# Kernel tuning notes

Hardware: AMD Instinct MI355X
Metric: run time of the kernel (lower is better)

Reference implementation:

```python
import jax, jax.numpy as jnp
import numpy as np

B, D, R = 16384, 4096, 64       # batch tokens, embed_dim, low_rank_dimension
N_PART = 8                       # number of subspace partitions
P = R // N_PART                  # partition size = 8
N_SEL = 4                        # partitions selected per example


def setup_inputs() -> dict:
    key = jax.random.key(0)
    k1, k2, k3, k4 = jax.random.split(key, 4)
    base = jax.random.normal(k1, (B, D), dtype=jnp.float32)
    source = jax.random.normal(k2, (B, D), dtype=jnp.float32)
    # orthogonal low-rank rotation (torch.nn.utils.parametrizations.orthogonal)
    W, _ = jnp.linalg.qr(jax.random.normal(k3, (D, R), dtype=jnp.float32))  # [D, R], orthonormal cols
    subspaces = jax.random.randint(k4, (B, N_SEL), 0, N_PART)               # partition ids per example
    return {"base": base, "source": source, "W": W, "subspaces": subspaces}


def reference(base, source, W, subspaces):
    # rotate into low-rank space: [B, R]
    rotated_base = base @ W
    rotated_source = source @ W
    diff = rotated_source - rotated_base

    # per-example selected rotated-space indices (contiguous partitions of size P)
    # idx[b] = concat over selected partitions of [p*P, p*P+P)
    idx = (subspaces[:, :, None] * P + jnp.arange(P)).reshape(B, N_SEL * P)  # [B, N_SEL*P]

    # Selecting columns of diff and matching rows of W.T, then matmul, is
    # equivalent to masking unselected rotated dims to zero and doing one GEMM.
    mask = jnp.zeros((B, R), dtype=diff.dtype).at[jnp.arange(B)[:, None], idx].set(1.0)
    output = base + (diff * mask) @ W.T  # [B, D]
    return output.astype(base.dtype)
```

## Files before the change

kernel.cpp:

```cpp
#include <hip/hip_runtime.h>


#define D_DIM 4096
#define R_DIM 64
#define BM    32
#define WAVESTG 16384
#define K1_SMEM 65536
#define OFF_RM  65536
#define FUSED_SMEM 70144

typedef short bf16vec8 __attribute__((ext_vector_type(8)));
typedef float f32x4v  __attribute__((ext_vector_type(4)));

#define VMWAIT(N)                                              \
  do {                                                         \
    asm volatile("s_waitcnt vmcnt(" #N ")" ::: "memory");      \
    __builtin_amdgcn_sched_barrier(0);                         \
  } while (0)

__device__ __forceinline__ unsigned int f2bf_u(float f) {
  unsigned int u = __builtin_bit_cast(unsigned int, f);
  return (u + 0x7fffu + ((u >> 16) & 1u)) >> 16;
}
__device__ __forceinline__ unsigned int pack2bf(float a, float b) {
  return f2bf_u(a) | (f2bf_u(b) << 16);
}
__device__ __forceinline__ void async_ld16(const void* g, void* l) {
  __builtin_amdgcn_global_load_lds(
      (const __attribute__((address_space(1))) void*)g,
      (__attribute__((address_space(3))) void*)l, 16, 0, 0);
}

__global__ __launch_bounds__(256)
void lrri_prep(const float* __restrict__ W, unsigned short* __restrict__ Wt,
               unsigned short* __restrict__ Wb) {
  const int idx = blockIdx.x * blockDim.x + threadIdx.x;
  const int k = idx >> 4;
  const int j = (idx & 15) * 4;
  float4 w = *(const float4*)(W + (size_t)k * R_DIM + j);
  ushort4 p;
  p.x = (unsigned short)f2bf_u(w.x);
  p.y = (unsigned short)f2bf_u(w.y);
  p.z = (unsigned short)f2bf_u(w.z);
  p.w = (unsigned short)f2bf_u(w.w);
  *(ushort4*)(Wb + (size_t)k * R_DIM + j) = p;
  Wt[(size_t)(j + 0) * D_DIM + k] = p.x;
  Wt[(size_t)(j + 1) * D_DIM + k] = p.y;
  Wt[(size_t)(j + 2) * D_DIM + k] = p.z;
  Wt[(size_t)(j + 3) * D_DIM + k] = p.w;
}

__global__ __launch_bounds__(256, 2)
void k1_rotdiff(const float* __restrict__ base, const float* __restrict__ srcp,
                const int* __restrict__ subs,
                const unsigned short* __restrict__ Wt_bf,
                unsigned short* __restrict__ rm_g)
{
  __shared__ __align__(16) unsigned char smem[K1_SMEM];
  const int tid  = threadIdx.x;
  const int wave = tid >> 6;
  const int lane = tid & 63;
  const int l4   = lane & 15;
  const int g    = lane >> 4;
  const int rh   = wave >> 1;
  const int kh   = wave & 1;
  const long rowbase = (long)blockIdx.x * BM;
  const long rowg    = rowbase + rh * 16;
  unsigned char* wbuf = smem + wave * WAVESTG;
  const int off1 = (blockIdx.x * 7) & 63;

  f32x4v acc[4];
  #pragma unroll
  for (int t = 0; t < 4; ++t) acc[t] = (f32x4v){0.f, 0.f, 0.f, 0.f};

  auto stage = [&](int c) {
    const int ch = (c + off1) & 63;
    unsigned char* buf = wbuf + (c & 1) * 8192;
    const long colf = kh * 2048 + ch * 32;
    #pragma unroll
    for (int q = 0; q < 2; ++q) {
      const int r = q * 8 + (lane >> 3);
      const unsigned b = ((unsigned)((lane & 7) * 16)) ^ ((unsigned)(r & 7) << 4);
      const long goff = (rowg + r) * (long)D_DIM + colf + (b >> 2);
      async_ld16(base + goff, buf + q * 1024);
    }
    #pragma unroll
    for (int q = 0; q < 2; ++q) {
      const int r = q * 8 + (lane >> 3);
      const unsigned b = ((unsigned)((lane & 7) * 16)) ^ ((unsigned)(r & 7) << 4);
      const long goff = (rowg + r) * (long)D_DIM + colf + (b >> 2);
      async_ld16(srcp + goff, buf + 2048 + q * 1024);
    }
    #pragma unroll
    for (int q = 0; q < 4; ++q) {
      const int j = q * 16 + (lane >> 2);
      const unsigned kb = ((unsigned)((lane & 3) * 16)) ^ ((unsigned)(j & 3) << 4);
      const char* src = (const char*)Wt_bf + (size_t)j * (D_DIM * 2) +
                        colf * 2 + kb;
      async_ld16(src, buf + 4096 + q * 1024);
    }
  };

  auto compute = [&](int c) {
    const unsigned char* buf = wbuf + (c & 1) * 8192;
    const unsigned sw = (unsigned)((l4 & 7) << 4);
    const unsigned c0 = ((unsigned)(g * 32)) ^ sw;
    const unsigned c1 = ((unsigned)(g * 32 + 16)) ^ sw;
    float4 fb0 = *(const float4*)(buf + l4 * 128 + c0);
    float4 fb1 = *(const float4*)(buf + l4 * 128 + c1);
    float4 fs0 = *(const float4*)(buf + 2048 + l4 * 128 + c0);
    float4 fs1 = *(const float4*)(buf + 2048 + l4 * 128 + c1);
    uint4 af;
    af.x = pack2bf(fs0.x - fb0.x, fs0.y - fb0.y);
    af.y = pack2bf(fs0.z - fb0.z, fs0.w - fb0.w);
    af.z = pack2bf(fs1.x - fb1.x, fs1.y - fb1.y);
    af.w = pack2bf(fs1.z - fb1.z, fs1.w - fb1.w);
    const unsigned wsl = ((unsigned)(g * 16)) ^ ((unsigned)(l4 & 3) << 4);
    #pragma unroll
    for (int t = 0; t < 4; ++t) {
      uint4 wf = *(const uint4*)(buf + 4096 + (t * 16 + l4) * 64 + wsl);
      acc[t] = __builtin_amdgcn_mfma_f32_16x16x32_bf16(
          __builtin_bit_cast(bf16vec8, af),
          __builtin_bit_cast(bf16vec8, wf), acc[t], 0, 0, 0);
    }
  };

  stage(0); stage(1);
  #pragma unroll 1
  for (int c = 0; c < 62; ++c) {
    VMWAIT(8);
    compute(c);
    __builtin_amdgcn_sched_barrier(0);
    stage(c + 2);
  }
  VMWAIT(8);
  compute(62);
  VMWAIT(0);
  compute(63);

  {
    float* part = (float*)wbuf;
    #pragma unroll
    for (int t = 0; t < 4; ++t)
      #pragma unroll
      for (int i = 0; i < 4; ++i)
        part[(g * 4 + i) * 72 + t * 16 + l4] = acc[t][i];
  }
  __syncthreads();

  {
    const int row = tid >> 3, jg = tid & 7;
    const int lr  = row & 15;
    const float* pa = (const float*)(smem + ((row >> 4) * 2 + 0) * WAVESTG);
    const float* pb = (const float*)(smem + ((row >> 4) * 2 + 1) * WAVESTG);
    int4 sb = *(const int4*)(subs + (rowbase + row) * 4);
    unsigned mbits = (1u << sb.x) | (1u << sb.y) | (1u << sb.z) | (1u << sb.w);
    unsigned short v[8];
    #pragma unroll
    for (int jj = 0; jj < 8; ++jj) {
      const int j = jg * 8 + jj;
      float sum = pa[lr * 72 + j] + pb[lr * 72 + j];
      v[jj] = ((mbits >> (j >> 3)) & 1u) ? (unsigned short)f2bf_u(sum)
                                         : (unsigned short)0;
    }
    uint4 pk;
    pk.x = (unsigned)v[0] | ((unsigned)v[1] << 16);
    pk.y = (unsigned)v[2] | ((unsigned)v[3] << 16);
    pk.z = (unsigned)v[4] | ((unsigned)v[5] << 16);
    pk.w = (unsigned)v[6] | ((unsigned)v[7] << 16);
    *(uint4*)(rm_g + (rowbase + row) * 64 + jg * 8) = pk;
  }
}

__global__ __launch_bounds__(256, 4)
void k2_apply(const float* __restrict__ base,
              const unsigned short* __restrict__ rm_g,
              const unsigned short* __restrict__ Wb_bf,
              float* __restrict__ out)
{
  __shared__ __align__(16) unsigned char smem[36864];
  const int tid  = threadIdx.x;
  const int wave = tid >> 6;
  const int lane = tid & 63;
  const int l4   = lane & 15;
  const int g    = lane >> 4;
  const long rowbase = (long)blockIdx.x * BM;
  const int off2 = (blockIdx.x * 5) & 15;

  uint4 a2[2][2];
  #pragma unroll
  for (int m = 0; m < 2; ++m)
    #pragma unroll
    for (int s = 0; s < 2; ++s)
      a2[m][s] = *(const uint4*)(rm_g + (rowbase + m * 16 + l4) * 64 +
                                 s * 32 + g * 8);

  float* cbuf = (float*)(smem + wave * 9216);
  #pragma unroll 1
  for (int grp = 0; grp < 16; ++grp) {
    const int ga = (grp + off2) & 15;
    const int cbase = wave * 1024 + ga * 64;
    float4 bb[8];
    #pragma unroll
    for (int v2 = 0; v2 < 8; ++v2) {
      const int r = g + v2 * 4;
      bb[v2] = *(const float4*)(base + (rowbase + r) * D_DIM + cbase + l4 * 4);
    }
    f32x4v a[2][4];
    #pragma unroll
    for (int m = 0; m < 2; ++m)
      #pragma unroll
      for (int t = 0; t < 4; ++t) a[m][t] = (f32x4v){0.f, 0.f, 0.f, 0.f};
    #pragma unroll
    for (int t = 0; t < 4; ++t) {
      #pragma unroll
      for (int s = 0; s < 2; ++s) {
        uint4 bfrag = *(const uint4*)(Wb_bf +
            (size_t)(cbase + t * 16 + l4) * R_DIM + s * 32 + g * 8);
        #pragma unroll
        for (int m = 0; m < 2; ++m)
          a[m][t] = __builtin_amdgcn_mfma_f32_16x16x32_bf16(
              __builtin_bit_cast(bf16vec8, a2[m][s]),
              __builtin_bit_cast(bf16vec8, bfrag), a[m][t], 0, 0, 0);
      }
    }
    #pragma unroll
    for (int m = 0; m < 2; ++m)
      #pragma unroll
      for (int t = 0; t < 4; ++t)
        #pragma unroll
        for (int i = 0; i < 4; ++i)
          cbuf[(m * 16 + g * 4 + i) * 72 + t * 16 + l4] = a[m][t][i];
    __syncthreads();
    #pragma unroll
    for (int v2 = 0; v2 < 8; ++v2) {
      const int r = g + v2 * 4;
      f32x4v cv = *(const f32x4v*)(cbuf + r * 72 + l4 * 4);
      float4 o;
      o.x = cv[0] + bb[v2].x;
      o.y = cv[1] + bb[v2].y;
      o.z = cv[2] + bb[v2].z;
      o.w = cv[3] + bb[v2].w;
      *(float4*)(out + (rowbase + r) * D_DIM + cbase + l4 * 4) = o;
    }
    __syncthreads();
  }
}

__global__ __launch_bounds__(256, 2)
void lrri_fused_nows(const float* __restrict__ base, const float* __restrict__ srcp,
                     const float* __restrict__ W, const int* __restrict__ subs,
                     float* __restrict__ out)
{
  __shared__ __align__(16) unsigned char smem[FUSED_SMEM];
  const int tid  = threadIdx.x;
  const int wave = tid >> 6;
  const int lane = tid & 63;
  const int l4   = lane & 15;
  const int g    = lane >> 4;
  const int rh   = wave >> 1;
  const int kh   = wave & 1;
  const long rowbase = (long)blockIdx.x * BM;
  const long rowg    = rowbase + rh * 16;
  unsigned char* wbuf = smem + wave * WAVESTG;
  const int off1 = (blockIdx.x * 7) & 63;
  const int off2 = (blockIdx.x * 5) & 15;

  f32x4v acc[4];
  #pragma unroll
  for (int t = 0; t < 4; ++t) acc[t] = (f32x4v){0.f, 0.f, 0.f, 0.f};

  #pragma unroll 1
  for (int c = 0; c < 64; ++c) {
    const int ch = (c + off1) & 63;
    unsigned char* buf = wbuf + (c & 1) * 8192;
    const long colf = kh * 2048 + ch * 32;
    #pragma unroll
    for (int q = 0; q < 2; ++q) {
      const int r = q * 8 + (lane >> 3);
      const unsigned b = ((unsigned)((lane & 7) * 16)) ^ ((unsigned)(r & 7) << 4);
      const long goff = (rowg + r) * (long)D_DIM + colf + (b >> 2);
      async_ld16(base + goff, buf + q * 1024);
      async_ld16(srcp + goff, buf + 2048 + q * 1024);
    }
    VMWAIT(0);
    const unsigned sw = (unsigned)((l4 & 7) << 4);
    const unsigned c0 = ((unsigned)(g * 32)) ^ sw;
    const unsigned c1 = ((unsigned)(g * 32 + 16)) ^ sw;
    float4 fb0 = *(const float4*)(buf + l4 * 128 + c0);
    float4 fb1 = *(const float4*)(buf + l4 * 128 + c1);
    float4 fs0 = *(const float4*)(buf + 2048 + l4 * 128 + c0);
    float4 fs1 = *(const float4*)(buf + 2048 + l4 * 128 + c1);
    uint4 af;
    af.x = pack2bf(fs0.x - fb0.x, fs0.y - fb0.y);
    af.y = pack2bf(fs0.z - fb0.z, fs0.w - fb0.w);
    af.z = pack2bf(fs1.x - fb1.x, fs1.y - fb1.y);
    af.w = pack2bf(fs1.z - fb1.z, fs1.w - fb1.w);
    #pragma unroll
    for (int t = 0; t < 4; ++t) {
      unsigned int pq[4];
      #pragma unroll
      for (int e2 = 0; e2 < 4; ++e2) {
        float wa = W[(size_t)(colf + g * 8 + e2 * 2    ) * R_DIM + t * 16 + l4];
        float wb = W[(size_t)(colf + g * 8 + e2 * 2 + 1) * R_DIM + t * 16 + l4];
        pq[e2] = pack2bf(wa, wb);
      }
      uint4 wf; wf.x = pq[0]; wf.y = pq[1]; wf.z = pq[2]; wf.w = pq[3];
      acc[t] = __builtin_amdgcn_mfma_f32_16x16x32_bf16(
          __builtin_bit_cast(bf16vec8, af),
          __builtin_bit_cast(bf16vec8, wf), acc[t], 0, 0, 0);
    }
  }

  {
    float* part = (float*)wbuf;
    #pragma unroll
    for (int t = 0; t < 4; ++t)
      #pragma unroll
      for (int i = 0; i < 4; ++i)
        part[(g * 4 + i) * 72 + t * 16 + l4] = acc[t][i];
  }
  __syncthreads();

  {
    const int row = tid >> 3, jg = tid & 7;
    const int lr  = row & 15;
    const float* pa = (const float*)(smem + ((row >> 4) * 2 + 0) * WAVESTG);
    const float* pb = (const float*)(smem + ((row >> 4) * 2 + 1) * WAVESTG);
    int4 sb = *(const int4*)(subs + (rowbase + row) * 4);
    unsigned mbits = (1u << sb.x) | (1u << sb.y) | (1u << sb.z) | (1u << sb.w);
    unsigned short v[8];
    #pragma unroll
    for (int jj = 0; jj < 8; ++jj) {
      const int j = jg * 8 + jj;
      float sum = pa[lr * 72 + j] + pb[lr * 72 + j];
      v[jj] = ((mbits >> (j >> 3)) & 1u) ? (unsigned short)f2bf_u(sum)
                                         : (unsigned short)0;
    }
    uint4 pk;
    pk.x = (unsigned)v[0] | ((unsigned)v[1] << 16);
    pk.y = (unsigned)v[2] | ((unsigned)v[3] << 16);
    pk.z = (unsigned)v[4] | ((unsigned)v[5] << 16);
    pk.w = (unsigned)v[6] | ((unsigned)v[7] << 16);
    *(uint4*)(smem + OFF_RM + row * 144 + jg * 16) = pk;
  }
  __syncthreads();

  uint4 a2[2][2];
  #pragma unroll
  for (int m = 0; m < 2; ++m)
    #pragma unroll
    for (int s = 0; s < 2; ++s)
      a2[m][s] = *(const uint4*)(smem + OFF_RM + (m * 16 + l4) * 144 +
                                 s * 64 + g * 16);
  float* cbuf = (float*)wbuf;
  #pragma unroll 1
  for (int grp = 0; grp < 16; ++grp) {
    const int ga = (grp + off2) & 15;
    const int cbase = wave * 1024 + ga * 64;
    float4 bb[8];
    #pragma unroll
    for (int v2 = 0; v2 < 8; ++v2) {
      const int r = g + v2 * 4;
      bb[v2] = *(const float4*)(base + (rowbase + r) * D_DIM + cbase + l4 * 4);
    }
    f32x4v a[2][4];
    #pragma unroll
    for (int m = 0; m < 2; ++m)
      #pragma unroll
      for (int t = 0; t < 4; ++t) a[m][t] = (f32x4v){0.f, 0.f, 0.f, 0.f};
    #pragma unroll
    for (int t = 0; t < 4; ++t) {
      #pragma unroll
      for (int s = 0; s < 2; ++s) {
        const float* wp = W + (size_t)(cbase + t * 16 + l4) * R_DIM + s * 32 + g * 8;
        float4 wa = *(const float4*)(wp);
        float4 wb2 = *(const float4*)(wp + 4);
        uint4 bfrag;
        bfrag.x = pack2bf(wa.x, wa.y); bfrag.y = pack2bf(wa.z, wa.w);
        bfrag.z = pack2bf(wb2.x, wb2.y); bfrag.w = pack2bf(wb2.z, wb2.w);
        #pragma unroll
        for (int m = 0; m < 2; ++m)
          a[m][t] = __builtin_amdgcn_mfma_f32_16x16x32_bf16(
              __builtin_bit_cast(bf16vec8, a2[m][s]),
              __builtin_bit_cast(bf16vec8, bfrag), a[m][t], 0, 0, 0);
      }
    }
    #pragma unroll
    for (int m = 0; m < 2; ++m)
      #pragma unroll
      for (int t = 0; t < 4; ++t)
        #pragma unroll
        for (int i = 0; i < 4; ++i)
          cbuf[(m * 16 + g * 4 + i) * 72 + t * 16 + l4] = a[m][t][i];
    #pragma unroll
    for (int v2 = 0; v2 < 8; ++v2) {
      const int r = g + v2 * 4;
      f32x4v cv = *(const f32x4v*)(cbuf + r * 72 + l4 * 4);
      float4 o;
      o.x = cv[0] + bb[v2].x;
      o.y = cv[1] + bb[v2].y;
      o.z = cv[2] + bb[v2].z;
      o.w = cv[3] + bb[v2].w;
      *(float4*)(out + (rowbase + r) * D_DIM + cbase + l4 * 4) = o;
    }
  }
}

extern "C" void kernel_launch(void* const* d_in, const int* in_sizes, int n_in,
                              void* d_out, int out_size, void* d_ws, size_t ws_size,
                              hipStream_t stream) {
  const float* base = (const float*)d_in[0];
  const float* srcp = (const float*)d_in[1];
  const float* W    = (const float*)d_in[2];
  const int*   subs = (const int*)d_in[3];
  float* out = (float*)d_out;

  const int nblocks = 16384 / BM;
  const size_t wconv = (size_t)2 * R_DIM * D_DIM * sizeof(unsigned short);
  const size_t rmsz  = (size_t)16384 * R_DIM * sizeof(unsigned short);
  if (d_ws && ws_size >= wconv + rmsz) {
    unsigned short* Wt = (unsigned short*)d_ws;
    unsigned short* Wb = Wt + (size_t)R_DIM * D_DIM;
    unsigned short* rm = Wb + (size_t)R_DIM * D_DIM;
    lrri_prep<<<256, 256, 0, stream>>>(W, Wt, Wb);
    k1_rotdiff<<<nblocks, 256, 0, stream>>>(base, srcp, subs, Wt, rm);
    k2_apply<<<nblocks, 256, 0, stream>>>(base, rm, Wb, out);
  } else {
    lrri_fused_nows<<<nblocks, 256, 0, stream>>>(base, srcp, W, subs, out);
  }
}
```

Baseline: 240.1 us.

## Rewrite rotdiff kernel with register-prefetched loads and 16-row blocks split over K

The first-stage kernel now handles 16 rows per block, with each of the four waves covering a quarter of the K dimension. It drops the LDS async-copy staging and loads base/source straight into registers with a two-deep software prefetch, and W fragments are read directly from global memory/L2. A small padded LDS buffer reduces the four wave partials. With far less shared memory, more blocks can be resident per CU (launch bounds raised to 3) and the latency of the memory-bound read of both inputs should be better hidden, at the cost of more global traffic for W fragments and more registers.

```diff
diff --git a/kernel.cpp b/kernel.cpp
--- a/kernel.cpp
+++ b/kernel.cpp
@@ -3,20 +3,11 @@
 
 #define D_DIM 4096
 #define R_DIM 64
-#define BM    32
-#define WAVESTG 16384
-#define K1_SMEM 65536
-#define OFF_RM  65536
-#define FUSED_SMEM 70144
+#define BM1   16
+#define BM2   32
 
 typedef short bf16vec8 __attribute__((ext_vector_type(8)));
 typedef float f32x4v  __attribute__((ext_vector_type(4)));
-
-#define VMWAIT(N)                                              \
-  do {                                                         \
-    asm volatile("s_waitcnt vmcnt(" #N ")" ::: "memory");      \
-    __builtin_amdgcn_sched_barrier(0);                         \
-  } while (0)
 
 __device__ __forceinline__ unsigned int f2bf_u(float f) {
   unsigned int u = __builtin_bit_cast(unsigned int, f);
@@ -50,13 +41,188 @@
   Wt[(size_t)(j + 3) * D_DIM + k] = p.w;
 }
 
-__global__ __launch_bounds__(256, 2)
+__global__ __launch_bounds__(256, 3)
 void k1_rotdiff(const float* __restrict__ base, const float* __restrict__ srcp,
                 const int* __restrict__ subs,
                 const unsigned short* __restrict__ Wt_bf,
                 unsigned short* __restrict__ rm_g)
 {
-  __shared__ __align__(16) unsigned char smem[K1_SMEM];
+  __shared__ __align__(16) float part[4][64 * 17];
+  const int tid  = threadIdx.x;
+  const int wave = tid >> 6;
+  const int lane = tid & 63;
+  const int l4   = lane & 15;
+  const int g    = lane >> 4;
+  const long rowbase = (long)blockIdx.x * BM1;
+  const long rowA    = (rowbase + l4) * (long)D_DIM;
+  const int  kq0     = wave * 1024;
+  const int  off1    = (blockIdx.x * 5) & 15;
+
+  f32x4v acc[4];
+  #pragma unroll
+  for (int t = 0; t < 4; ++t) acc[t] = (f32x4v){0.f, 0.f, 0.f, 0.f};
+
+  auto loadd = [&](int c, float4 (&vb)[4], float4 (&vs)[4]) {
+    const int ch = (c + off1) & 15;
+    const long colf = kq0 + ch * 64;
+    #pragma unroll
+    for (int q = 0; q < 4; ++q) {
+      const long off = rowA + colf + (q >> 1) * 32 + g * 8 + (q & 1) * 4;
+      vb[q] = *(const float4*)(base + off);
+      vs[q] = *(const float4*)(srcp + off);
+    }
+  };
+
+  auto comp = [&](int c, const float4 (&vb)[4], const float4 (&vs)[4]) {
+    const int ch = (c + off1) & 15;
+    const long colf = kq0 + ch * 64;
+    uint4 df[2];
+    #pragma unroll
+    for (int s = 0; s < 2; ++s) {
+      float d0 = vs[s*2].x - vb[s*2].x, d1 = vs[s*2].y - vb[s*2].y;
+      float d2 = vs[s*2].z - vb[s*2].z, d3 = vs[s*2].w - vb[s*2].w;
+      float d4 = vs[s*2+1].x - vb[s*2+1].x, d5 = vs[s*2+1].y - vb[s*2+1].y;
+      float d6 = vs[s*2+1].z - vb[s*2+1].z, d7 = vs[s*2+1].w - vb[s*2+1].w;
+      df[s].x = pack2bf(d0, d1);
+      df[s].y = pack2bf(d2, d3);
+      df[s].z = pack2bf(d4, d5);
+      df[s].w = pack2bf(d6, d7);
+    }
+    #pragma unroll
+    for (int t = 0; t < 4; ++t) {
+      #pragma unroll
+      for (int s = 0; s < 2; ++s) {
+        uint4 wf = *(const uint4*)(Wt_bf + (size_t)(t * 16 + l4) * D_DIM +
+                                   colf + s * 32 + g * 8);
+        acc[t] = __builtin_amdgcn_mfma_f32_16x16x32_bf16(
+            __builtin_bit_cast(bf16vec8, wf),
+            __builtin_bit_cast(bf16vec8, df[s]),
+            acc[t], 0, 0, 0);
+      }
+    }
+  };
+
+  float4 b0[4], s0[4], b1[4], s1[4];
+  loadd(0, b0, s0);
+  #pragma unroll 1
+  for (int cc = 0; cc < 14; cc += 2) {
+    loadd(cc + 1, b1, s1);
+    comp(cc, b0, s0);
+    loadd(cc + 2, b0, s0);
+    comp(cc + 1, b1, s1);
+  }
+  loadd(15, b1, s1);
+  comp(14, b0, s0);
+  comp(15, b1, s1);
+
+  #pragma unroll
+  for (int t = 0; t < 4; ++t)
+    #pragma unroll
+    for (int i = 0; i < 4; ++i)
+      part[wave][(t * 16 + g * 4 + i) * 17 + l4] = acc[t][i];
+  __syncthreads();
+
+  {
+    const int row = tid >> 4, jg = tid & 15;
+    int4 sb = *(const int4*)(subs + (rowbase + row) * 4);
+    unsigned mbits = (1u << sb.x) | (1u << sb.y) | (1u << sb.z) | (1u << sb.w);
+    unsigned short v[4];
+    #pragma unroll
+    for (int jj = 0; jj < 4; ++jj) {
+      const int j = jg * 4 + jj;
+      float sum = part[0][j * 17 + row] + part[1][j * 17 + row] +
+                  part[2][j * 17 + row] + part[3][j * 17 + row];
+      v[jj] = ((mbits >> (j >> 3)) & 1u) ? (unsigned short)f2bf_u(sum)
+                                         : (unsigned short)0;
+    }
+    uint2 pk;
+    pk.x = (unsigned)v[0] | ((unsigned)v[1] << 16);
+    pk.y = (unsigned)v[2] | ((unsigned)v[3] << 16);
+    *(uint2*)(rm_g + (rowbase + row) * 64 + jg * 4) = pk;
+  }
+}
+
+__global__ __launch_bounds__(256, 4)
+void k2_apply(const float* __restrict__ base,
+              const unsigned short* __restrict__ rm_g,
+              const unsigned short* __restrict__ Wb_bf,
+              float* __restrict__ out)
+{
+  __shared__ __align__(16) unsigned char smem[36864];
+  const int tid  = threadIdx.x;
+  const int wave = tid >> 6;
+  const int lane = tid & 63;
+  const int l4   = lane & 15;
+  const int g    = lane >> 4;
+  const long rowbase = (long)blockIdx.x * BM2;
+  const int off2 = (blockIdx.x * 5) & 15;
+
+  uint4 a2[2][2];
+  #pragma unroll
+  for (int m = 0; m < 2; ++m)
+    #pragma unroll
+    for (int s = 0; s < 2; ++s)
+      a2[m][s] = *(const uint4*)(rm_g + (rowbase + m * 16 + l4) * 64 +
+                                 s * 32 + g * 8);
+
+  float* cbuf = (float*)(smem + wave * 9216);
+  #pragma unroll 1
+  for (int grp = 0; grp < 16; ++grp) {
+    const int ga = (grp + off2) & 15;
+    const int cbase = wave * 1024 + ga * 64;
+    float4 bb[8];
+    #pragma unroll
+    for (int v2 = 0; v2 < 8; ++v2) {
+      const int r = g + v2 * 4;
+      bb[v2] = *(const float4*)(base + (rowbase + r) * D_DIM + cbase + l4 * 4);
+    }
+    f32x4v a[2][4];
+    #pragma unroll
+    for (int m = 0; m < 2; ++m)
+      #pragma unroll
+      for (int t = 0; t < 4; ++t) a[m][t] = (f32x4v){0.f, 0.f, 0.f, 0.f};
+    #pragma unroll
+    for (int t = 0; t < 4; ++t) {
+      #pragma unroll
+      for (int s = 0; s < 2; ++s) {
+        uint4 bfrag = *(const uint4*)(Wb_bf +
+            (size_t)(cbase + t * 16 + l4) * R_DIM + s * 32 + g * 8);
+        #pragma unroll
+        for (int m = 0; m < 2; ++m)
+          a[m][t] = __builtin_amdgcn_mfma_f32_16x16x32_bf16(
+              __builtin_bit_cast(bf16vec8, a2[m][s]),
+              __builtin_bit_cast(bf16vec8, bfrag), a[m][t], 0, 0, 0);
+      }
+    }
+    #pragma unroll
+    for (int m = 0; m < 2; ++m)
+      #pragma unroll
+      for (int t = 0; t < 4; ++t)
+        #pragma unroll
+        for (int i = 0; i < 4; ++i)
+          cbuf[(m * 16 + g * 4 + i) * 72 + t * 16 + l4] = a[m][t][i];
+    __syncthreads();
+    #pragma unroll
+    for (int v2 = 0; v2 < 8; ++v2) {
+      const int r = g + v2 * 4;
+      f32x4v cv = *(const f32x4v*)(cbuf + r * 72 + l4 * 4);
+      float4 o;
+      o.x = cv[0] + bb[v2].x;
+      o.y = cv[1] + bb[v2].y;
+      o.z = cv[2] + bb[v2].z;
+      o.w = cv[3] + bb[v2].w;
+      *(float4*)(out + (rowbase + r) * D_DIM + cbase + l4 * 4) = o;
+    }
+    __syncthreads();
+  }
+}
+
+__global__ __launch_bounds__(256, 2)
+void lrri_fused_nows(const float* __restrict__ base, const float* __restrict__ srcp,
+                     const float* __restrict__ W, const int* __restrict__ subs,
+                     float* __restrict__ out)
+{
+  __shared__ __align__(16) unsigned char smem[70144];
   const int tid  = threadIdx.x;
   const int wave = tid >> 6;
   const int lane = tid & 63;
@@ -64,16 +230,18 @@
   const int g    = lane >> 4;
   const int rh   = wave >> 1;
   const int kh   = wave & 1;
-  const long rowbase = (long)blockIdx.x * BM;
+  const long rowbase = (long)blockIdx.x * BM2;
   const long rowg    = rowbase + rh * 16;
-  unsigned char* wbuf = smem + wave * WAVESTG;
+  unsigned char* wbuf = smem + wave * 16384;
   const int off1 = (blockIdx.x * 7) & 63;
+  const int off2 = (blockIdx.x * 5) & 15;
 
   f32x4v acc[4];
   #pragma unroll
   for (int t = 0; t < 4; ++t) acc[t] = (f32x4v){0.f, 0.f, 0.f, 0.f};
 
-  auto stage = [&](int c) {
+  #pragma unroll 1
+  for (int c = 0; c < 64; ++c) {
     const int ch = (c + off1) & 63;
     unsigned char* buf = wbuf + (c & 1) * 8192;
     const long colf = kh * 2048 + ch * 32;
@@ -83,26 +251,10 @@
       const unsigned b = ((unsigned)((lane & 7) * 16)) ^ ((unsigned)(r & 7) << 4);
       const long goff = (rowg + r) * (long)D_DIM + colf + (b >> 2);
       async_ld16(base + goff, buf + q * 1024);
-    }
-    #pragma unroll
-    for (int q = 0; q < 2; ++q) {
-      const int r = q * 8 + (lane >> 3);
-      const unsigned b = ((unsigned)((lane & 7) * 16)) ^ ((unsigned)(r & 7) << 4);
-      const long goff = (rowg + r) * (long)D_DIM + colf + (b >> 2);
       async_ld16(srcp + goff, buf + 2048 + q * 1024);
     }
-    #pragma unroll
-    for (int q = 0; q < 4; ++q) {
-      const int j = q * 16 + (lane >> 2);
-      const unsigned kb = ((unsigned)((lane & 3) * 16)) ^ ((unsigned)(j & 3) << 4);
-      const char* src = (const char*)Wt_bf + (size_t)j * (D_DIM * 2) +
-                        colf * 2 + kb;
-      async_ld16(src, buf + 4096 + q * 1024);
-    }
-  };
-
-  auto compute = [&](int c) {
-    const unsigned char* buf = wbuf + (c & 1) * 8192;
+    asm volatile("s_waitcnt vmcnt(0)" ::: "memory");
+    __builtin_amdgcn_sched_barrier(0);
     const unsigned sw = (unsigned)((l4 & 7) << 4);
     const unsigned c0 = ((unsigned)(g * 32)) ^ sw;
     const unsigned c1 = ((unsigned)(g * 32 + 16)) ^ sw;
@@ -115,187 +267,6 @@
     af.y = pack2bf(fs0.z - fb0.z, fs0.w - fb0.w);
     af.z = pack2bf(fs1.x - fb1.x, fs1.y - fb1.y);
     af.w = pack2bf(fs1.z - fb1.z, fs1.w - fb1.w);
-    const unsigned wsl = ((unsigned)(g * 16)) ^ ((unsigned)(l4 & 3) << 4);
-    #pragma unroll
-    for (int t = 0; t < 4; ++t) {
-      uint4 wf = *(const uint4*)(buf + 4096 + (t * 16 + l4) * 64 + wsl);
-      acc[t] = __builtin_amdgcn_mfma_f32_16x16x32_bf16(
-          __builtin_bit_cast(bf16vec8, af),
-          __builtin_bit_cast(bf16vec8, wf), acc[t], 0, 0, 0);
-    }
-  };
-
-  stage(0); stage(1);
-  #pragma unroll 1
-  for (int c = 0; c < 62; ++c) {
-    VMWAIT(8);
-    compute(c);
-    __builtin_amdgcn_sched_barrier(0);
-    stage(c + 2);
-  }
-  VMWAIT(8);
-  compute(62);
-  VMWAIT(0);
-  compute(63);
-
-  {
-    float* part = (float*)wbuf;
-    #pragma unroll
-    for (int t = 0; t < 4; ++t)
-      #pragma unroll
-      for (int i = 0; i < 4; ++i)
-        part[(g * 4 + i) * 72 + t * 16 + l4] = acc[t][i];
-  }
-  __syncthreads();
-
-  {
-    const int row = tid >> 3, jg = tid & 7;
-    const int lr  = row & 15;
-    const float* pa = (const float*)(smem + ((row >> 4) * 2 + 0) * WAVESTG);
-    const float* pb = (const float*)(smem + ((row >> 4) * 2 + 1) * WAVESTG);
-    int4 sb = *(const int4*)(subs + (rowbase + row) * 4);
-    unsigned mbits = (1u << sb.x) | (1u << sb.y) | (1u << sb.z) | (1u << sb.w);
-    unsigned short v[8];
-    #pragma unroll
-    for (int jj = 0; jj < 8; ++jj) {
-      const int j = jg * 8 + jj;
-      float sum = pa[lr * 72 + j] + pb[lr * 72 + j];
-      v[jj] = ((mbits >> (j >> 3)) & 1u) ? (unsigned short)f2bf_u(sum)
-                                         : (unsigned short)0;
-    }
-    uint4 pk;
-    pk.x = (unsigned)v[0] | ((unsigned)v[1] << 16);
-    pk.y = (unsigned)v[2] | ((unsigned)v[3] << 16);
-    pk.z = (unsigned)v[4] | ((unsigned)v[5] << 16);
-    pk.w = (unsigned)v[6] | ((unsigned)v[7] << 16);
-    *(uint4*)(rm_g + (rowbase + row) * 64 + jg * 8) = pk;
-  }
-}
-
-__global__ __launch_bounds__(256, 4)
-void k2_apply(const float* __restrict__ base,
-              const unsigned short* __restrict__ rm_g,
-              const unsigned short* __restrict__ Wb_bf,
-              float* __restrict__ out)
-{
-  __shared__ __align__(16) unsigned char smem[36864];
-  const int tid  = threadIdx.x;
-  const int wave = tid >> 6;
-  const int lane = tid & 63;
-  const int l4   = lane & 15;
-  const int g    = lane >> 4;
-  const long rowbase = (long)blockIdx.x * BM;
-  const int off2 = (blockIdx.x * 5) & 15;
-
-  uint4 a2[2][2];
-  #pragma unroll
-  for (int m = 0; m < 2; ++m)
-    #pragma unroll
-    for (int s = 0; s < 2; ++s)
-      a2[m][s] = *(const uint4*)(rm_g + (rowbase + m * 16 + l4) * 64 +
-                                 s * 32 + g * 8);
-
-  float* cbuf = (float*)(smem + wave * 9216);
-  #pragma unroll 1
-  for (int grp = 0; grp < 16; ++grp) {
-    const int ga = (grp + off2) & 15;
-    const int cbase = wave * 1024 + ga * 64;
-    float4 bb[8];
-    #pragma unroll
-    for (int v2 = 0; v2 < 8; ++v2) {
-      const int r = g + v2 * 4;
-      bb[v2] = *(const float4*)(base + (rowbase + r) * D_DIM + cbase + l4 * 4);
-    }
-    f32x4v a[2][4];
-    #pragma unroll
-    for (int m = 0; m < 2; ++m)
-      #pragma unroll
-      for (int t = 0; t < 4; ++t) a[m][t] = (f32x4v){0.f, 0.f, 0.f, 0.f};
-    #pragma unroll
-    for (int t = 0; t < 4; ++t) {
-      #pragma unroll
-      for (int s = 0; s < 2; ++s) {
-        uint4 bfrag = *(const uint4*)(Wb_bf +
-            (size_t)(cbase + t * 16 + l4) * R_DIM + s * 32 + g * 8);
-        #pragma unroll
-        for (int m = 0; m < 2; ++m)
-          a[m][t] = __builtin_amdgcn_mfma_f32_16x16x32_bf16(
-              __builtin_bit_cast(bf16vec8, a2[m][s]),
-              __builtin_bit_cast(bf16vec8, bfrag), a[m][t], 0, 0, 0);
-      }
-    }
-    #pragma unroll
-    for (int m = 0; m < 2; ++m)
-      #pragma unroll
-      for (int t = 0; t < 4; ++t)
-        #pragma unroll
-        for (int i = 0; i < 4; ++i)
-          cbuf[(m * 16 + g * 4 + i) * 72 + t * 16 + l4] = a[m][t][i];
-    __syncthreads();
-    #pragma unroll
-    for (int v2 = 0; v2 < 8; ++v2) {
-      const int r = g + v2 * 4;
-      f32x4v cv = *(const f32x4v*)(cbuf + r * 72 + l4 * 4);
-      float4 o;
-      o.x = cv[0] + bb[v2].x;
-      o.y = cv[1] + bb[v2].y;
-      o.z = cv[2] + bb[v2].z;
-      o.w = cv[3] + bb[v2].w;
-      *(float4*)(out + (rowbase + r) * D_DIM + cbase + l4 * 4) = o;
-    }
-    __syncthreads();
-  }
-}
-
-__global__ __launch_bounds__(256, 2)
-void lrri_fused_nows(const float* __restrict__ base, const float* __restrict__ srcp,
-                     const float* __restrict__ W, const int* __restrict__ subs,
-                     float* __restrict__ out)
-{
-  __shared__ __align__(16) unsigned char smem[FUSED_SMEM];
-  const int tid  = threadIdx.x;
-  const int wave = tid >> 6;
-  const int lane = tid & 63;
-  const int l4   = lane & 15;
-  const int g    = lane >> 4;
-  const int rh   = wave >> 1;
-  const int kh   = wave & 1;
-  const long rowbase = (long)blockIdx.x * BM;
-  const long rowg    = rowbase + rh * 16;
-  unsigned char* wbuf = smem + wave * WAVESTG;
-  const int off1 = (blockIdx.x * 7) & 63;
-  const int off2 = (blockIdx.x * 5) & 15;
-
-  f32x4v acc[4];
-  #pragma unroll
-  for (int t = 0; t < 4; ++t) acc[t] = (f32x4v){0.f, 0.f, 0.f, 0.f};
-
-  #pragma unroll 1
-  for (int c = 0; c < 64; ++c) {
-    const int ch = (c + off1) & 63;
-    unsigned char* buf = wbuf + (c & 1) * 8192;
-    const long colf = kh * 2048 + ch * 32;
-    #pragma unroll
-    for (int q = 0; q < 2; ++q) {
-      const int r = q * 8 + (lane >> 3);
-      const unsigned b = ((unsigned)((lane & 7) * 16)) ^ ((unsigned)(r & 7) << 4);
-      const long goff = (rowg + r) * (long)D_DIM + colf + (b >> 2);
-      async_ld16(base + goff, buf + q * 1024);
-      async_ld16(srcp + goff, buf + 2048 + q * 1024);
-    }
-    VMWAIT(0);
-    const unsigned sw = (unsigned)((l4 & 7) << 4);
-    const unsigned c0 = ((unsigned)(g * 32)) ^ sw;
-    const unsigned c1 = ((unsigned)(g * 32 + 16)) ^ sw;
-    float4 fb0 = *(const float4*)(buf + l4 * 128 + c0);
-    float4 fb1 = *(const float4*)(buf + l4 * 128 + c1);
-    float4 fs0 = *(const float4*)(buf + 2048 + l4 * 128 + c0);
-    float4 fs1 = *(const float4*)(buf + 2048 + l4 * 128 + c1);
-    uint4 af;
-    af.x = pack2bf(fs0.x - fb0.x, fs0.y - fb0.y);
-    af.y = pack2bf(fs0.z - fb0.z, fs0.w - fb0.w);
-    af.z = pack2bf(fs1.x - fb1.x, fs1.y - fb1.y);
-    af.w = pack2bf(fs1.z - fb1.z, fs1.w - fb1.w);
     #pragma unroll
     for (int t = 0; t < 4; ++t) {
       unsigned int pq[4];
@@ -325,8 +296,8 @@
   {
     const int row = tid >> 3, jg = tid & 7;
     const int lr  = row & 15;
-    const float* pa = (const float*)(smem + ((row >> 4) * 2 + 0) * WAVESTG);
-    const float* pb = (const float*)(smem + ((row >> 4) * 2 + 1) * WAVESTG);
+    const float* pa = (const float*)(smem + ((row >> 4) * 2 + 0) * 16384);
+    const float* pb = (const float*)(smem + ((row >> 4) * 2 + 1) * 16384);
     int4 sb = *(const int4*)(subs + (rowbase + row) * 4);
     unsigned mbits = (1u << sb.x) | (1u << sb.y) | (1u << sb.z) | (1u << sb.w);
     unsigned short v[8];
@@ -342,7 +313,7 @@
     pk.y = (unsigned)v[2] | ((unsigned)v[3] << 16);
     pk.z = (unsigned)v[4] | ((unsigned)v[5] << 16);
     pk.w = (unsigned)v[6] | ((unsigned)v[7] << 16);
-    *(uint4*)(smem + OFF_RM + row * 144 + jg * 16) = pk;
+    *(uint4*)(smem + 65536 + row * 144 + jg * 16) = pk;
   }
   __syncthreads();
 
@@ -351,7 +322,7 @@
   for (int m = 0; m < 2; ++m)
     #pragma unroll
     for (int s = 0; s < 2; ++s)
-      a2[m][s] = *(const uint4*)(smem + OFF_RM + (m * 16 + l4) * 144 +
+      a2[m][s] = *(const uint4*)(smem + 65536 + (m * 16 + l4) * 144 +
                                  s * 64 + g * 16);
   float* cbuf = (float*)wbuf;
   #pragma unroll 1
@@ -416,7 +387,6 @@
   const int*   subs = (const int*)d_in[3];
   float* out = (float*)d_out;
 
-  const int nblocks = 16384 / BM;
   const size_t wconv = (size_t)2 * R_DIM * D_DIM * sizeof(unsigned short);
   const size_t rmsz  = (size_t)16384 * R_DIM * sizeof(unsigned short);
   if (d_ws && ws_size >= wconv + rmsz) {
@@ -424,9 +394,9 @@
     unsigned short* Wb = Wt + (size_t)R_DIM * D_DIM;
     unsigned short* rm = Wb + (size_t)R_DIM * D_DIM;
     lrri_prep<<<256, 256, 0, stream>>>(W, Wt, Wb);
-    k1_rotdiff<<<nblocks, 256, 0, stream>>>(base, srcp, subs, Wt, rm);
-    k2_apply<<<nblocks, 256, 0, stream>>>(base, rm, Wb, out);
+    k1_rotdiff<<<16384 / BM1, 256, 0, stream>>>(base, srcp, subs, Wt, rm);
+    k2_apply<<<16384 / BM2, 256, 0, stream>>>(base, rm, Wb, out);
   } else {
-    lrri_fused_nows<<<nblocks, 256, 0, stream>>>(base, srcp, W, subs, out);
-  }
-}
+    lrri_fused_nows<<<16384 / BM2, 256, 0, stream>>>(base, srcp, W, subs, out);
+  }
+}
```

New measurement: 263.3 us. 1.1x slower.
